# Performance work log

Hardware: AMD Instinct MI355X
Metric: run time of the kernel (lower is better)

## Reference

```python
import jax, jax.numpy as jnp
import numpy as np

# Tsit5 Butcher tableau (Tsitouras 2011), same coefficients diffrax uses.
C2, C3, C4, C5, C6 = 0.161, 0.327, 0.9, 0.9800255409045097, 1.0
A21 = 0.161
A31, A32 = -0.008480655492356989, 0.335480655492357
A41, A42, A43 = 2.8971530571054935, -6.359448489975075, 4.3622954328695815
A51, A52, A53, A54 = 5.325864828439257, -11.748883564062828, 7.4955393428898365, -0.09249506636175525
A61, A62, A63, A64, A65 = 5.86145544294642, -12.92096931784711, 8.159367898576159, -0.071584973281401, -0.028269050394068383
B1, B2, B3, B4, B5, B6 = 0.09646076681806523, 0.01, 0.4798896504144996, 1.379008574103742, -3.290069515436081, 2.324710524099774

DIM, WIDTH, DEPTH = 64, 256, 3
BATCH, NT = 4096, 101


def setup_inputs() -> dict:
    key = jax.random.key(0)
    ks = jax.random.split(key, 10)
    ts = jnp.linspace(0.0, 1.0, NT, dtype=jnp.float32)
    y0 = jax.random.normal(ks[0], (BATCH, DIM), dtype=jnp.float32)
    def lin(k, fan_in, fan_out):
        lim = 1.0 / np.sqrt(fan_in)
        kw, kb = jax.random.split(k)
        W = jax.random.uniform(kw, (fan_in, fan_out), jnp.float32, -lim, lim)
        b = jax.random.uniform(kb, (fan_out,), jnp.float32, -lim, lim)
        return W, b
    W0, b0 = lin(ks[1], DIM, WIDTH)
    W1, b1 = lin(ks[2], WIDTH, WIDTH)
    W2, b2 = lin(ks[3], WIDTH, WIDTH)
    W3, b3 = lin(ks[4], WIDTH, DIM)
    return {"ts": ts, "y0": y0, "W0": W0, "b0": b0, "W1": W1, "b1": b1,
            "W2": W2, "b2": b2, "W3": W3, "b3": b3}


def _vf(y, W0, b0, W1, b1, W2, b2, W3, b3):
    # MLP vector field f(t, y) = MLP(y); tanh hidden activations, depth=3 hidden layers.
    h = jnp.tanh(y @ W0 + b0)
    h = jnp.tanh(h @ W1 + b1)
    h = jnp.tanh(h @ W2 + b2)
    return h @ W3 + b3


def reference(ts, y0, W0, b0, W1, b1, W2, b2, W3, b3):
    f = lambda y: _vf(y, W0, b0, W1, b1, W2, b2, W3, b3)

    def tsit5_step(y, h):
        # h: scalar step size (broadcasts over [batch, dim])
        k1 = f(y)
        k2 = f(y + h * (A21 * k1))
        k3 = f(y + h * (A31 * k1 + A32 * k2))
        k4 = f(y + h * (A41 * k1 + A42 * k2 + A43 * k3))
        k5 = f(y + h * (A51 * k1 + A52 * k2 + A53 * k3 + A54 * k4))
        k6 = f(y + h * (A61 * k1 + A62 * k2 + A63 * k3 + A64 * k4 + A65 * k5))
        return y + h * (B1 * k1 + B2 * k2 + B3 * k3 + B4 * k4 + B5 * k5 + B6 * k6)

    def scan_body(y, hpair):
        y_new = tsit5_step(y, hpair)
        return y_new, y_new

    hs = ts[1:] - ts[:-1]                     # [NT-1] step sizes between save points
    hs = hs[:, None, None]                    # broadcast to [NT-1, 1, 1]
    _, ys_tail = jax.lax.scan(scan_body, y0, hs)
    return jnp.concatenate([y0[None], ys_tail], axis=0)  # [NT, batch, dim]
```

## Files before the change

kernel.cpp:

```cpp
#include <hip/hip_runtime.h>

#define NTIME   101
#define BATCH   4096
#define DIM     64
#define WIDTH   256
#define TB      16
#define NTHREADS 1024
#define AST     264
#define SPS     68

#define A21 0.161f
#define A31 (-0.008480655492356989f)
#define A32 0.335480655492357f
#define A41 2.8971530571054935f
#define A42 (-6.359448489975075f)
#define A43 4.3622954328695815f
#define A51 5.325864828439257f
#define A52 (-11.748883564062828f)
#define A53 7.4955393428898365f
#define A54 (-0.09249506636175525f)
#define A61 5.86145544294642f
#define A62 (-12.92096931784711f)
#define A63 8.159367898576159f
#define A64 (-0.071584973281401f)
#define A65 (-0.028269050394068383f)
#define B1 0.09646076681806523f
#define B2 0.01f
#define B3 0.4798896504144996f
#define B4 1.379008574103742f
#define B5 (-3.290069515436081f)
#define B6 2.324710524099774f

typedef float  floatx4 __attribute__((ext_vector_type(4)));
typedef _Float16 halfx8 __attribute__((ext_vector_type(8)));

#define L0S1 0
#define L0S2 16384
#define L1S1 32768
#define L1S2 98304
#define L2S1 163840
#define L2S2 229376
#define L3S1 294912
#define L3S2 311296

__device__ __forceinline__ float fast_tanh(float x) {
    float e = __expf(2.0f * x);
    return 1.0f - 2.0f / (e + 1.0f);
}

__device__ __forceinline__ void bar_lds() {
    asm volatile("s_waitcnt lgkmcnt(0)\n\ts_barrier" ::: "memory");
}

__global__ void pack_weights(const float* __restrict__ W0, const float* __restrict__ W1,
                             const float* __restrict__ W2, const float* __restrict__ W3,
                             _Float16* __restrict__ ws)
{
    int idx = blockIdx.x * 256 + threadIdx.x;
    const float* W; int K, N, e; size_t d1, d2;
    if (idx < 16384)       { W = W0; K = 64;  N = 256; e = idx;          d1 = L0S1; d2 = L0S2; }
    else if (idx < 81920)  { W = W1; K = 256; N = 256; e = idx - 16384;  d1 = L1S1; d2 = L1S2; }
    else if (idx < 147456) { W = W2; K = 256; N = 256; e = idx - 81920;  d1 = L2S1; d2 = L2S2; }
    else if (idx < 163840) { W = W3; K = 256; N = 64;  e = idx - 147456; d1 = L3S1; d2 = L3S2; }
    else return;
    int k = e / N, n = e % N;
    float w = W[e];
    _Float16 h1 = (_Float16)w;
    _Float16 h2 = (_Float16)((w - (float)h1) * 4096.0f);
    int kc = k >> 5, q = (k >> 3) & 3, j = k & 7, nt = n >> 4, nc = n & 15;
    size_t off = ((size_t)((nt * (K / 32) + kc) * 64 + q * 16 + nc)) * 8 + j;
    ws[d1 + off] = h1;
    ws[d2 + off] = h2;
}

template<int KCNT>
__device__ __forceinline__ void mfma_run(const _Float16* __restrict__ pA1,
                                         const _Float16* __restrict__ pA2,
                                         const _Float16* __restrict__ B1g,
                                         const _Float16* __restrict__ B2g,
                                         int fbBase, int kcStart, int lane,
                                         floatx4& acc1o, floatx4& acc2o)
{
    const int m = lane & 15, q = lane >> 4;
    floatx4 acc1 = (floatx4)0.0f, acc2 = (floatx4)0.0f;
    halfx8 va1[2], va2[2], vb1[2], vb2[2];

    const int aOff0 = m * AST + kcStart * 32 + q * 8;
    const size_t fOff0 = ((size_t)fbBase * 64 + lane) * 8;
    vb1[0] = *(const halfx8*)(B1g + fOff0);
    vb2[0] = *(const halfx8*)(B2g + fOff0);
    va1[0] = *(const halfx8*)(pA1 + aOff0);
    va2[0] = *(const halfx8*)(pA2 + aOff0);

    #pragma unroll
    for (int i = 0; i < KCNT; ++i) {
        const int cur = i & 1, nxt = cur ^ 1;
        if (i + 1 < KCNT) {
            const size_t fOff = ((size_t)(fbBase + i + 1) * 64 + lane) * 8;
            vb1[nxt] = *(const halfx8*)(B1g + fOff);
            vb2[nxt] = *(const halfx8*)(B2g + fOff);
            const int aOff = m * AST + (kcStart + i + 1) * 32 + q * 8;
            va1[nxt] = *(const halfx8*)(pA1 + aOff);
            va2[nxt] = *(const halfx8*)(pA2 + aOff);
        }
        acc1 = __builtin_amdgcn_mfma_f32_16x16x32_f16(va1[cur], vb1[cur], acc1, 0, 0, 0);
        acc2 = __builtin_amdgcn_mfma_f32_16x16x32_f16(va1[cur], vb2[cur], acc2, 0, 0, 0);
        acc2 = __builtin_amdgcn_mfma_f32_16x16x32_f16(va2[cur], vb1[cur], acc2, 0, 0, 0);
    }
    acc1o = acc1; acc2o = acc2;
}

__device__ __forceinline__ void hidden_epi(floatx4 a1, floatx4 a2,
                                           const float* __restrict__ bias,
                                           _Float16* __restrict__ o1,
                                           _Float16* __restrict__ o2,
                                           int w, int lane)
{
    const int m = lane & 15, q = lane >> 4;
    const int col = (w << 4) + m;
    const float bb = bias[col];
    #pragma unroll
    for (int v = 0; v < 4; ++v) {
        float val = fast_tanh(a1[v] + a2[v] * (1.0f / 4096.0f) + bb);
        _Float16 h1 = (_Float16)val;
        _Float16 h2 = (_Float16)((val - (float)h1) * 4096.0f);
        const int idx = (q * 4 + v) * AST + col;
        o1[idx] = h1;
        o2[idx] = h2;
    }
}

__global__ void __launch_bounds__(NTHREADS)
ode_kernel(const float* __restrict__ ts, const float* __restrict__ y0,
           const float* __restrict__ b0, const float* __restrict__ b1,
           const float* __restrict__ b2, const float* __restrict__ b3,
           const _Float16* __restrict__ ws, float* __restrict__ out)
{
    __shared__ __align__(16) _Float16 sA1[2][TB * AST];
    __shared__ __align__(16) _Float16 sA2[2][TB * AST];
    __shared__ __align__(16) float sK[5][TB * DIM];
    __shared__ __align__(16) float sY[TB * DIM];
    __shared__ __align__(16) float sP[4][TB * SPS];
    __shared__ __align__(16) float sBias[832];

    const int tid  = threadIdx.x;
    const int lane = tid & 63;
    const int w    = tid >> 6;
    const long base = (long)blockIdx.x * (TB * DIM);
    const int c = tid & 63;
    const int r = tid >> 6;

    if (tid < 832) {
        float v;
        if (tid < 256)      v = b0[tid];
        else if (tid < 512) v = b1[tid - 256];
        else if (tid < 768) v = b2[tid - 512];
        else                v = b3[tid - 768];
        sBias[tid] = v;
    }
    {
        float v = y0[base + tid];
        sY[tid] = v;
        __builtin_nontemporal_store(v, &out[base + tid]);
        _Float16 h1 = (_Float16)v;
        _Float16 h2 = (_Float16)((v - (float)h1) * 4096.0f);
        sA1[0][r * AST + c] = h1;
        sA2[0][r * AST + c] = h2;
    }
    __syncthreads();

    const int r68 = r * SPS + c;

    for (int t = 0; t < NTIME - 1; ++t) {
        const float h = ts[t + 1] - ts[t];

        #pragma unroll 1
        for (int s = 0; s < 6; ++s) {
            floatx4 a1, a2;
            mfma_run<2>(sA1[0], sA2[0], ws + L0S1, ws + L0S2, w * 2, 0, lane, a1, a2);
            hidden_epi(a1, a2, sBias + 0, sA1[1], sA2[1], w, lane);
            bar_lds();
            mfma_run<8>(sA1[1], sA2[1], ws + L1S1, ws + L1S2, w * 8, 0, lane, a1, a2);
            hidden_epi(a1, a2, sBias + 256, sA1[0], sA2[0], w, lane);
            bar_lds();
            mfma_run<8>(sA1[0], sA2[0], ws + L2S1, ws + L2S2, w * 8, 0, lane, a1, a2);
            hidden_epi(a1, a2, sBias + 512, sA1[1], sA2[1], w, lane);
            bar_lds();
            {
                const int nt = w & 3, kg = w >> 2;
                mfma_run<2>(sA1[1], sA2[1], ws + L3S1, ws + L3S2,
                            nt * 8 + kg * 2, kg * 2, lane, a1, a2);
                const int m = lane & 15, q = lane >> 4;
                #pragma unroll
                for (int v = 0; v < 4; ++v)
                    sP[kg][(q * 4 + v) * SPS + nt * 16 + m]
                        = a1[v] + a2[v] * (1.0f / 4096.0f);
            }
            bar_lds();

            float kv = sP[0][r68] + sP[1][r68] + sP[2][r68] + sP[3][r68]
                     + sBias[768 + c];
            float v;
            if (s == 0) {
                sK[0][tid] = kv;
                v = fmaf(h, A21 * kv, sY[tid]);
            } else if (s == 1) {
                sK[1][tid] = kv;
                v = fmaf(h, fmaf(A31, sK[0][tid], A32 * kv), sY[tid]);
            } else if (s == 2) {
                sK[2][tid] = kv;
                float sum = A41 * sK[0][tid] + A42 * sK[1][tid] + A43 * kv;
                v = fmaf(h, sum, sY[tid]);
            } else if (s == 3) {
                sK[3][tid] = kv;
                float sum = A51 * sK[0][tid] + A52 * sK[1][tid] + A53 * sK[2][tid] + A54 * kv;
                v = fmaf(h, sum, sY[tid]);
            } else if (s == 4) {
                sK[4][tid] = kv;
                float sum = A61 * sK[0][tid] + A62 * sK[1][tid] + A63 * sK[2][tid]
                          + A64 * sK[3][tid] + A65 * kv;
                v = fmaf(h, sum, sY[tid]);
            } else {
                float sum = B1 * sK[0][tid] + B2 * sK[1][tid] + B3 * sK[2][tid]
                          + B4 * sK[3][tid] + B5 * sK[4][tid] + B6 * kv;
                v = fmaf(h, sum, sY[tid]);
                sY[tid] = v;
                __builtin_nontemporal_store(v, &out[(long)(t + 1) * (BATCH * DIM) + base + tid]);
            }
            _Float16 h1 = (_Float16)v;
            _Float16 h2 = (_Float16)((v - (float)h1) * 4096.0f);
            sA1[0][r * AST + c] = h1;
            sA2[0][r * AST + c] = h2;
            bar_lds();
        }
    }
}

extern "C" void kernel_launch(void* const* d_in, const int* in_sizes, int n_in,
                              void* d_out, int out_size, void* d_ws, size_t ws_size,
                              hipStream_t stream) {
    (void)in_sizes; (void)n_in; (void)ws_size; (void)out_size;
    const float* ts = (const float*)d_in[0];
    const float* y0 = (const float*)d_in[1];
    const float* W0 = (const float*)d_in[2];
    const float* b0 = (const float*)d_in[3];
    const float* W1 = (const float*)d_in[4];
    const float* b1 = (const float*)d_in[5];
    const float* W2 = (const float*)d_in[6];
    const float* b2 = (const float*)d_in[7];
    const float* W3 = (const float*)d_in[8];
    const float* b3 = (const float*)d_in[9];
    _Float16* ws = (_Float16*)d_ws;
    float* out = (float*)d_out;

    hipLaunchKernelGGL(pack_weights, dim3(640), dim3(256), 0, stream, W0, W1, W2, W3, ws);
    hipLaunchKernelGGL(ode_kernel, dim3(BATCH / TB), dim3(NTHREADS), 0, stream,
                       ts, y0, b0, b1, b2, b3, ws, out);
}
```

Measured before the change: 4.545 ms.

## Cache W0/W3 hi-split in LDS and merge last layer with RK stage update

Copies the fp16 high-part slices of W0 and W3 into shared memory once per block, so the first and last layers read weights from LDS instead of global memory. The last layer now runs on only 4 waves, each covering the full K range, so the split-K partial-sum buffer and one barrier per stage go away. The Runge-Kutta stage update is fused into that epilogue, with each lane handling 4 rows. The trade-off is that 12 of 16 waves sit idle during layer 3, and the larger LDS footprint may limit occupancy.

```diff
diff --git a/kernel.cpp b/kernel.cpp
--- a/kernel.cpp
+++ b/kernel.cpp
@@ -7,7 +7,7 @@
 #define TB      16
 #define NTHREADS 1024
 #define AST     264
-#define SPS     68
+#define SKS     68
 
 #define A21 0.161f
 #define A31 (-0.008480655492356989f)
@@ -138,17 +138,26 @@
 {
     __shared__ __align__(16) _Float16 sA1[2][TB * AST];
     __shared__ __align__(16) _Float16 sA2[2][TB * AST];
-    __shared__ __align__(16) float sK[5][TB * DIM];
-    __shared__ __align__(16) float sY[TB * DIM];
-    __shared__ __align__(16) float sP[4][TB * SPS];
+    __shared__ __align__(16) _Float16 cW0[32768];
+    __shared__ __align__(16) _Float16 cW3[16384];
+    __shared__ __align__(16) float sK[5][TB * SKS];
+    __shared__ __align__(16) float sY[TB * SKS];
     __shared__ __align__(16) float sBias[832];
 
     const int tid  = threadIdx.x;
     const int lane = tid & 63;
     const int w    = tid >> 6;
+    const int m    = lane & 15, q = lane >> 4;
     const long base = (long)blockIdx.x * (TB * DIM);
     const int c = tid & 63;
     const int r = tid >> 6;
+
+    #pragma unroll
+    for (int i = 0; i < 4; ++i)
+        ((halfx8*)cW0)[tid + i * NTHREADS] = ((const halfx8*)(ws + L0S1))[tid + i * NTHREADS];
+    #pragma unroll
+    for (int i = 0; i < 2; ++i)
+        ((halfx8*)cW3)[tid + i * NTHREADS] = ((const halfx8*)(ws + L3S1))[tid + i * NTHREADS];
 
     if (tid < 832) {
         float v;
@@ -160,7 +169,7 @@
     }
     {
         float v = y0[base + tid];
-        sY[tid] = v;
+        sY[r * SKS + c] = v;
         __builtin_nontemporal_store(v, &out[base + tid]);
         _Float16 h1 = (_Float16)v;
         _Float16 h2 = (_Float16)((v - (float)h1) * 4096.0f);
@@ -169,15 +178,13 @@
     }
     __syncthreads();
 
-    const int r68 = r * SPS + c;
-
     for (int t = 0; t < NTIME - 1; ++t) {
         const float h = ts[t + 1] - ts[t];
 
         #pragma unroll 1
         for (int s = 0; s < 6; ++s) {
             floatx4 a1, a2;
-            mfma_run<2>(sA1[0], sA2[0], ws + L0S1, ws + L0S2, w * 2, 0, lane, a1, a2);
+            mfma_run<2>(sA1[0], sA2[0], cW0, cW0 + 16384, w * 2, 0, lane, a1, a2);
             hidden_epi(a1, a2, sBias + 0, sA1[1], sA2[1], w, lane);
             bar_lds();
             mfma_run<8>(sA1[1], sA2[1], ws + L1S1, ws + L1S2, w * 8, 0, lane, a1, a2);
@@ -186,51 +193,74 @@
             mfma_run<8>(sA1[0], sA2[0], ws + L2S1, ws + L2S2, w * 8, 0, lane, a1, a2);
             hidden_epi(a1, a2, sBias + 512, sA1[1], sA2[1], w, lane);
             bar_lds();
-            {
-                const int nt = w & 3, kg = w >> 2;
-                mfma_run<2>(sA1[1], sA2[1], ws + L3S1, ws + L3S2,
-                            nt * 8 + kg * 2, kg * 2, lane, a1, a2);
-                const int m = lane & 15, q = lane >> 4;
+            if (w < 4) {
+                mfma_run<8>(sA1[1], sA2[1], cW3, ws + L3S2, w * 8, 0, lane, a1, a2);
+                const int col3 = (w << 4) + m;
+                const float bb3 = sBias[768 + col3];
+                float kv[4], vn[4];
                 #pragma unroll
                 for (int v = 0; v < 4; ++v)
-                    sP[kg][(q * 4 + v) * SPS + nt * 16 + m]
-                        = a1[v] + a2[v] * (1.0f / 4096.0f);
+                    kv[v] = a1[v] + a2[v] * (1.0f / 4096.0f) + bb3;
+
+                if (s == 0) {
+                    #pragma unroll
+                    for (int v = 0; v < 4; ++v) {
+                        const int ri = (q * 4 + v) * SKS + col3;
+                        sK[0][ri] = kv[v];
+                        vn[v] = fmaf(h, A21 * kv[v], sY[ri]);
+                    }
+                } else if (s == 1) {
+                    #pragma unroll
+                    for (int v = 0; v < 4; ++v) {
+                        const int ri = (q * 4 + v) * SKS + col3;
+                        sK[1][ri] = kv[v];
+                        vn[v] = fmaf(h, fmaf(A31, sK[0][ri], A32 * kv[v]), sY[ri]);
+                    }
+                } else if (s == 2) {
+                    #pragma unroll
+                    for (int v = 0; v < 4; ++v) {
+                        const int ri = (q * 4 + v) * SKS + col3;
+                        sK[2][ri] = kv[v];
+                        vn[v] = fmaf(h, A41 * sK[0][ri] + A42 * sK[1][ri] + A43 * kv[v], sY[ri]);
+                    }
+                } else if (s == 3) {
+                    #pragma unroll
+                    for (int v = 0; v < 4; ++v) {
+                        const int ri = (q * 4 + v) * SKS + col3;
+                        sK[3][ri] = kv[v];
+                        vn[v] = fmaf(h, A51 * sK[0][ri] + A52 * sK[1][ri]
+                                      + A53 * sK[2][ri] + A54 * kv[v], sY[ri]);
+                    }
+                } else if (s == 4) {
+                    #pragma unroll
+                    for (int v = 0; v < 4; ++v) {
+                        const int ri = (q * 4 + v) * SKS + col3;
+                        sK[4][ri] = kv[v];
+                        vn[v] = fmaf(h, A61 * sK[0][ri] + A62 * sK[1][ri] + A63 * sK[2][ri]
+                                      + A64 * sK[3][ri] + A65 * kv[v], sY[ri]);
+                    }
+                } else {
+                    #pragma unroll
+                    for (int v = 0; v < 4; ++v) {
+                        const int ri = (q * 4 + v) * SKS + col3;
+                        float sum = B1 * sK[0][ri] + B2 * sK[1][ri] + B3 * sK[2][ri]
+                                  + B4 * sK[3][ri] + B5 * sK[4][ri] + B6 * kv[v];
+                        vn[v] = fmaf(h, sum, sY[ri]);
+                        sY[ri] = vn[v];
+                        __builtin_nontemporal_store(vn[v],
+                            &out[(long)(t + 1) * (BATCH * DIM) + base
+                                 + (q * 4 + v) * 64 + col3]);
+                    }
+                }
+                #pragma unroll
+                for (int v = 0; v < 4; ++v) {
+                    _Float16 h1 = (_Float16)vn[v];
+                    _Float16 h2 = (_Float16)((vn[v] - (float)h1) * 4096.0f);
+                    const int idx = (q * 4 + v) * AST + col3;
+                    sA1[0][idx] = h1;
+                    sA2[0][idx] = h2;
+                }
             }
-            bar_lds();
-
-            float kv = sP[0][r68] + sP[1][r68] + sP[2][r68] + sP[3][r68]
-                     + sBias[768 + c];
-            float v;
-            if (s == 0) {
-                sK[0][tid] = kv;
-                v = fmaf(h, A21 * kv, sY[tid]);
-            } else if (s == 1) {
-                sK[1][tid] = kv;
-                v = fmaf(h, fmaf(A31, sK[0][tid], A32 * kv), sY[tid]);
-            } else if (s == 2) {
-                sK[2][tid] = kv;
-                float sum = A41 * sK[0][tid] + A42 * sK[1][tid] + A43 * kv;
-                v = fmaf(h, sum, sY[tid]);
-            } else if (s == 3) {
-                sK[3][tid] = kv;
-                float sum = A51 * sK[0][tid] + A52 * sK[1][tid] + A53 * sK[2][tid] + A54 * kv;
-                v = fmaf(h, sum, sY[tid]);
-            } else if (s == 4) {
-                sK[4][tid] = kv;
-                float sum = A61 * sK[0][tid] + A62 * sK[1][tid] + A63 * sK[2][tid]
-                          + A64 * sK[3][tid] + A65 * kv;
-                v = fmaf(h, sum, sY[tid]);
-            } else {
-                float sum = B1 * sK[0][tid] + B2 * sK[1][tid] + B3 * sK[2][tid]
-                          + B4 * sK[3][tid] + B5 * sK[4][tid] + B6 * kv;
-                v = fmaf(h, sum, sY[tid]);
-                sY[tid] = v;
-                __builtin_nontemporal_store(v, &out[(long)(t + 1) * (BATCH * DIM) + base + tid]);
-            }
-            _Float16 h1 = (_Float16)v;
-            _Float16 h2 = (_Float16)((v - (float)h1) * 4096.0f);
-            sA1[0][r * AST + c] = h1;
-            sA2[0][r * AST + c] = h2;
             bar_lds();
         }
     }
```

Measured after the change: 5.449 ms. +19.9%, slower.

## Stream MFMA weight fragments through per-wave LDS double buffer via global_load_lds

Applied to the files above, without the earlier changes.

Replaces direct global-to-register loads of the split-fp16 weight fragments with asynchronous global_load_lds copies into a per-wave two-slot LDS ring. The next layer's first two fragments are prefetched across the epilogue and barrier so weight latency overlaps compute, with manual vmcnt waits gating consumption. This adds 64KB of LDS per block and relies on hand-written s_waitcnt counts staying correct against the compiler's other memory ops. That is fragile, since the epilogue or other global loads could shift the counters.

```diff
diff --git a/kernel.cpp b/kernel.cpp
--- a/kernel.cpp
+++ b/kernel.cpp
@@ -73,39 +73,55 @@
     ws[d2 + off] = h2;
 }
 
+__device__ __forceinline__ void stage_b(const _Float16* __restrict__ g1,
+                                        const _Float16* __restrict__ g2,
+                                        _Float16* slot, int fb, int lane)
+{
+    const _Float16* s1 = g1 + (((size_t)fb) * 64 + lane) * 8;
+    const _Float16* s2 = g2 + (((size_t)fb) * 64 + lane) * 8;
+    __builtin_amdgcn_global_load_lds(
+        (const __attribute__((address_space(1))) void*)s1,
+        (__attribute__((address_space(3))) void*)slot, 16, 0, 0);
+    __builtin_amdgcn_global_load_lds(
+        (const __attribute__((address_space(1))) void*)s2,
+        (__attribute__((address_space(3))) void*)(slot + 512), 16, 0, 0);
+}
+
 template<int KCNT>
-__device__ __forceinline__ void mfma_run(const _Float16* __restrict__ pA1,
-                                         const _Float16* __restrict__ pA2,
-                                         const _Float16* __restrict__ B1g,
-                                         const _Float16* __restrict__ B2g,
-                                         int fbBase, int kcStart, int lane,
-                                         floatx4& acc1o, floatx4& acc2o)
+__device__ __forceinline__ void mfma_staged(const _Float16* __restrict__ pA1,
+                                            const _Float16* __restrict__ pA2,
+                                            const _Float16* __restrict__ g1,
+                                            const _Float16* __restrict__ g2,
+                                            _Float16* slot, int fbBase, int kcStart,
+                                            int lane,
+                                            floatx4& acc1o, floatx4& acc2o)
 {
     const int m = lane & 15, q = lane >> 4;
     floatx4 acc1 = (floatx4)0.0f, acc2 = (floatx4)0.0f;
-    halfx8 va1[2], va2[2], vb1[2], vb2[2];
+    halfx8 va1[2], va2[2];
 
     const int aOff0 = m * AST + kcStart * 32 + q * 8;
-    const size_t fOff0 = ((size_t)fbBase * 64 + lane) * 8;
-    vb1[0] = *(const halfx8*)(B1g + fOff0);
-    vb2[0] = *(const halfx8*)(B2g + fOff0);
     va1[0] = *(const halfx8*)(pA1 + aOff0);
     va2[0] = *(const halfx8*)(pA2 + aOff0);
 
     #pragma unroll
     for (int i = 0; i < KCNT; ++i) {
         const int cur = i & 1, nxt = cur ^ 1;
+        if (i + 1 < KCNT) asm volatile("s_waitcnt vmcnt(2)" ::: "memory");
+        else              asm volatile("s_waitcnt vmcnt(0)" ::: "memory");
+        const _Float16* bs = slot + cur * 1024;
+        halfx8 vb1 = *(const halfx8*)(bs + lane * 8);
+        halfx8 vb2 = *(const halfx8*)(bs + 512 + lane * 8);
         if (i + 1 < KCNT) {
-            const size_t fOff = ((size_t)(fbBase + i + 1) * 64 + lane) * 8;
-            vb1[nxt] = *(const halfx8*)(B1g + fOff);
-            vb2[nxt] = *(const halfx8*)(B2g + fOff);
             const int aOff = m * AST + (kcStart + i + 1) * 32 + q * 8;
             va1[nxt] = *(const halfx8*)(pA1 + aOff);
             va2[nxt] = *(const halfx8*)(pA2 + aOff);
         }
-        acc1 = __builtin_amdgcn_mfma_f32_16x16x32_f16(va1[cur], vb1[cur], acc1, 0, 0, 0);
-        acc2 = __builtin_amdgcn_mfma_f32_16x16x32_f16(va1[cur], vb2[cur], acc2, 0, 0, 0);
-        acc2 = __builtin_amdgcn_mfma_f32_16x16x32_f16(va2[cur], vb1[cur], acc2, 0, 0, 0);
+        acc1 = __builtin_amdgcn_mfma_f32_16x16x32_f16(va1[cur], vb1, acc1, 0, 0, 0);
+        acc2 = __builtin_amdgcn_mfma_f32_16x16x32_f16(va1[cur], vb2, acc2, 0, 0, 0);
+        acc2 = __builtin_amdgcn_mfma_f32_16x16x32_f16(va2[cur], vb1, acc2, 0, 0, 0);
+        if (i + 2 < KCNT)
+            stage_b(g1, g2, slot + cur * 1024, fbBase + i + 2, lane);
     }
     acc1o = acc1; acc2o = acc2;
 }
@@ -138,6 +154,7 @@
 {
     __shared__ __align__(16) _Float16 sA1[2][TB * AST];
     __shared__ __align__(16) _Float16 sA2[2][TB * AST];
+    __shared__ __align__(16) _Float16 sB[16 * 2048];
     __shared__ __align__(16) float sK[5][TB * DIM];
     __shared__ __align__(16) float sY[TB * DIM];
     __shared__ __align__(16) float sP[4][TB * SPS];
@@ -149,6 +166,8 @@
     const long base = (long)blockIdx.x * (TB * DIM);
     const int c = tid & 63;
     const int r = tid >> 6;
+    _Float16* slot = sB + w * 2048;
+    const int nt = w & 3, kg = w >> 2;
 
     if (tid < 832) {
         float v;
@@ -169,6 +188,9 @@
     }
     __syncthreads();
 
+    stage_b(ws + L0S1, ws + L0S2, slot,        w * 2,     lane);
+    stage_b(ws + L0S1, ws + L0S2, slot + 1024, w * 2 + 1, lane);
+
     const int r68 = r * SPS + c;
 
     for (int t = 0; t < NTIME - 1; ++t) {
@@ -177,19 +199,29 @@
         #pragma unroll 1
         for (int s = 0; s < 6; ++s) {
             floatx4 a1, a2;
-            mfma_run<2>(sA1[0], sA2[0], ws + L0S1, ws + L0S2, w * 2, 0, lane, a1, a2);
+            mfma_staged<2>(sA1[0], sA2[0], ws + L0S1, ws + L0S2, slot,
+                           w * 2, 0, lane, a1, a2);
+            stage_b(ws + L1S1, ws + L1S2, slot,        w * 8,     lane);
+            stage_b(ws + L1S1, ws + L1S2, slot + 1024, w * 8 + 1, lane);
             hidden_epi(a1, a2, sBias + 0, sA1[1], sA2[1], w, lane);
             bar_lds();
-            mfma_run<8>(sA1[1], sA2[1], ws + L1S1, ws + L1S2, w * 8, 0, lane, a1, a2);
+            mfma_staged<8>(sA1[1], sA2[1], ws + L1S1, ws + L1S2, slot,
+                           w * 8, 0, lane, a1, a2);
+            stage_b(ws + L2S1, ws + L2S2, slot,        w * 8,     lane);
+            stage_b(ws + L2S1, ws + L2S2, slot + 1024, w * 8 + 1, lane);
             hidden_epi(a1, a2, sBias + 256, sA1[0], sA2[0], w, lane);
             bar_lds();
-            mfma_run<8>(sA1[0], sA2[0], ws + L2S1, ws + L2S2, w * 8, 0, lane, a1, a2);
+            mfma_staged<8>(sA1[0], sA2[0], ws + L2S1, ws + L2S2, slot,
+                           w * 8, 0, lane, a1, a2);
+            stage_b(ws + L3S1, ws + L3S2, slot,        nt * 8 + kg * 2,     lane);
+            stage_b(ws + L3S1, ws + L3S2, slot + 1024, nt * 8 + kg * 2 + 1, lane);
             hidden_epi(a1, a2, sBias + 512, sA1[1], sA2[1], w, lane);
             bar_lds();
             {
-                const int nt = w & 3, kg = w >> 2;
-                mfma_run<2>(sA1[1], sA2[1], ws + L3S1, ws + L3S2,
-                            nt * 8 + kg * 2, kg * 2, lane, a1, a2);
+                mfma_staged<2>(sA1[1], sA2[1], ws + L3S1, ws + L3S2, slot,
+                               nt * 8 + kg * 2, kg * 2, lane, a1, a2);
+                stage_b(ws + L0S1, ws + L0S2, slot,        w * 2,     lane);
+                stage_b(ws + L0S1, ws + L0S2, slot + 1024, w * 2 + 1, lane);
                 const int m = lane & 15, q = lane >> 4;
                 #pragma unroll
                 for (int v = 0; v < 4; ++v)
```

After: 4.760 ms. 4.7% more time.
